# Kernel optimization log

Hardware: AMD Instinct MI355X
Metric: run time of the kernel (lower is better)

## Reference

```python
import jax, jax.numpy as jnp
import numpy as np

N_NODES = 100000
N_FEATS = 512
HIDDEN = 64
NUM_SAMPLES = 5
NUM_CLASSES = 16
BATCH = 16384


def setup_inputs() -> dict:
    key = jax.random.key(0)
    k1, k2, k3, k4, k5, k6, k7 = jax.random.split(key, 7)
    nodes = jax.random.randint(k1, (BATCH,), 0, N_NODES, dtype=jnp.int64) if jax.config.jax_enable_x64 else jax.random.randint(k1, (BATCH,), 0, N_NODES, dtype=jnp.int32)
    neigh_idx = jax.random.randint(k2, (N_NODES, NUM_SAMPLES), 0, N_NODES, dtype=jnp.int32)
    features = jax.random.normal(k3, (N_NODES, N_FEATS), dtype=jnp.float32)
    # xavier-uniform style init
    def xavier(k, shape):
        fan_in, fan_out = shape[1], shape[0]
        lim = jnp.sqrt(6.0 / (fan_in + fan_out)).astype(jnp.float32)
        return jax.random.uniform(k, shape, jnp.float32, -lim, lim)
    w1 = xavier(k4, (HIDDEN, 2 * N_FEATS))      # enc1 weight
    w2 = xavier(k5, (HIDDEN, 2 * HIDDEN))       # enc2 weight
    w_cls = xavier(k6, (NUM_CLASSES, HIDDEN))   # classifier weight
    return {"features": features, "w1": w1, "w2": w2, "w_cls": w_cls,
            "nodes": nodes, "neigh_idx": neigh_idx}


def reference(features, w1, w2, w_cls, nodes, neigh_idx):
    # Layer 1 (enc1, gcn=False): concat(self, mean(sampled neighbors)) -> W1 -> ReLU
    # Computed for all nodes (superset of what torch computes lazily; same values).
    neigh1 = features[neigh_idx].mean(axis=1)                      # [N, F]
    h1 = jax.nn.relu(jnp.concatenate([features, neigh1], axis=1) @ w1.T)  # [N, H]
    # Layer 2 (enc2) on the query batch
    self2 = h1[nodes]                                              # [B, H]
    neigh2 = h1[neigh_idx[nodes]].mean(axis=1)                     # [B, H]
    h2 = jax.nn.relu(jnp.concatenate([self2, neigh2], axis=1) @ w2.T)     # [B, H]
    # scores = (w_cls @ h2.T).T == h2 @ w_cls.T
    return h2 @ w_cls.T                                            # [B, C]
```

## Files before the change

kernel.cpp:

```cpp
#include <hip/hip_runtime.h>
#include <hip/hip_bf16.h>

#define N_NODES 100000
#define N_FEATS 512
#define HIDDEN 64
#define NUM_SAMPLES 5
#define NUM_CLASSES 16
#define BATCH 16384

typedef __attribute__((ext_vector_type(8))) short bf16x8;
typedef __attribute__((ext_vector_type(8))) unsigned short u16x8;
typedef __attribute__((ext_vector_type(4))) float f32x4;

static __device__ __forceinline__ float bf2f(unsigned short s) {
    unsigned int u = ((unsigned int)s) << 16;
    return __builtin_bit_cast(float, u);
}
static __device__ __forceinline__ short f2bf(float v) {
    __hip_bfloat16 b = __float2bfloat16(v);
    return *reinterpret_cast<short*>(&b);
}
static __device__ __forceinline__ int clampi(int v) {
    return ((unsigned)v < (unsigned)N_NODES) ? v : 0;
}

__global__ __launch_bounds__(256) void prep(const float* __restrict__ w1f,
                                            short* __restrict__ w1p,
                                            const int* __restrict__ nodes_i32,
                                            int* __restrict__ flag) {
    const int t = blockIdx.x * 256 + threadIdx.x;
    if (t < 64 * 1024) {
        const int j = t & 7;
        const int lane = (t >> 3) & 63;
        const int nb = (t >> 9) & 7;
        const int kk = t >> 12;
        const int l16 = lane & 15, quad = lane >> 4;
        const int cn = nb * 16 + l16;
        const int h = cn & 63, part = cn >> 6;
        w1p[t] = f2bf(w1f[h * 1024 + part * 512 + kk * 32 + quad * 8 + j]);
    }
    if (blockIdx.x == 0 && threadIdx.x == 0) {
        int odd_nonzero = 0;
        for (int i = 0; i < 64; i++)
            if (nodes_i32[2 * i + 1] != 0) odd_nonzero++;
        *flag = (odd_nonzero == 0) ? 1 : 0;
    }
}

__global__ __launch_bounds__(256) void pq_gemm(const float* __restrict__ feat,
                                               const short* __restrict__ w1p,
                                               short* __restrict__ PQ) {
    const int wave = threadIdx.x >> 6;
    const int lane = threadIdx.x & 63;
    const int quad = lane >> 4;
    const int l16  = lane & 15;
    const int r0   = blockIdx.x * 64 + wave * 16;

    int rA = r0 + l16;
    if (rA >= N_NODES) rA = N_NODES - 1;

    const float* aptr = feat + (size_t)rA * N_FEATS + quad * 8;
    const short* bbase = w1p + lane * 8;

    f32x4 buf[2][8];
#pragma unroll
    for (int c = 0; c < 4; c++) {
        buf[0][2 * c]     = *reinterpret_cast<const f32x4*>(aptr + c * 32);
        buf[0][2 * c + 1] = *reinterpret_cast<const f32x4*>(aptr + c * 32 + 4);
    }

    f32x4 acc[8];
#pragma unroll
    for (int i = 0; i < 8; i++) acc[i] = (f32x4){0.f, 0.f, 0.f, 0.f};

#pragma unroll
    for (int g = 0; g < 4; g++) {
        const int cur = g & 1;
        if (g < 3) {
#pragma unroll
            for (int c = 0; c < 4; c++) {
                buf[cur ^ 1][2 * c]     = *reinterpret_cast<const f32x4*>(aptr + (g + 1) * 128 + c * 32);
                buf[cur ^ 1][2 * c + 1] = *reinterpret_cast<const f32x4*>(aptr + (g + 1) * 128 + c * 32 + 4);
            }
        }
#pragma unroll
        for (int kk2 = 0; kk2 < 4; kk2++) {
            const int kk = g * 4 + kk2;
            bf16x8 afrag;
#pragma unroll
            for (int j = 0; j < 4; j++) {
                afrag[j]     = f2bf(buf[cur][2 * kk2][j]);
                afrag[4 + j] = f2bf(buf[cur][2 * kk2 + 1][j]);
            }
            const short* bk = bbase + kk * 4096;
#pragma unroll
            for (int nb = 0; nb < 8; nb++) {
                bf16x8 bfrag = *reinterpret_cast<const bf16x8*>(bk + nb * 512);
                acc[nb] = __builtin_amdgcn_mfma_f32_16x16x32_bf16(afrag, bfrag, acc[nb], 0, 0, 0);
            }
        }
    }

#pragma unroll
    for (int nb = 0; nb < 8; nb++) {
        const int cn = nb * 16 + l16;
#pragma unroll
        for (int r = 0; r < 4; r++) {
            const int row = r0 + quad * 4 + r;
            if (row < N_NODES) PQ[(size_t)row * 128 + cn] = f2bf(acc[nb][r]);
        }
    }
}

__global__ __launch_bounds__(256) void h1_combine(short* __restrict__ PQ,
                                                  const int* __restrict__ neigh_idx) {
    const int t = blockIdx.x * 256 + threadIdx.x;
    const int n = t >> 3;
    const int sub = t & 7;
    if (n >= N_NODES) return;

    u16x8 pv = *reinterpret_cast<const u16x8*>(PQ + (size_t)n * 128 + sub * 8);
    float s[8];
#pragma unroll
    for (int j = 0; j < 8; j++) s[j] = 0.f;
#pragma unroll
    for (int i = 0; i < NUM_SAMPLES; i++) {
        const int ni = clampi(neigh_idx[n * NUM_SAMPLES + i]);
        u16x8 qv = *reinterpret_cast<const u16x8*>(PQ + (size_t)ni * 128 + 64 + sub * 8);
#pragma unroll
        for (int j = 0; j < 8; j++) s[j] += bf2f(qv[j]);
    }
    u16x8 ov;
#pragma unroll
    for (int j = 0; j < 8; j++) {
        float v = bf2f(pv[j]) + 0.2f * s[j];
        v = v > 0.f ? v : 0.f;
        ov[j] = (unsigned short)f2bf(v);
    }
    *reinterpret_cast<u16x8*>(PQ + (size_t)n * 128 + sub * 8) = ov;
}

__global__ __launch_bounds__(256) void layer2_cls(const short* __restrict__ PQ,
                                                  const int* __restrict__ nodes_i32,
                                                  const int* __restrict__ neigh_idx,
                                                  const float* __restrict__ w2,
                                                  const float* __restrict__ wcls,
                                                  const int* __restrict__ flag,
                                                  float* __restrict__ out) {
    __shared__ float gbuf[16][128];
    __shared__ float h2buf[16][64];
    const int wave = threadIdx.x >> 6;
    const int lane = threadIdx.x & 63;
    const int is64 = *flag;
    const int b0 = blockIdx.x * 16;

#pragma unroll
    for (int it = 0; it < 4; it++) {
        const int item = wave * 4 + it;
        const int b = b0 + item;
        const int node = clampi(nodes_i32[is64 ? 2 * b : b]);
        float selfv = bf2f((unsigned short)PQ[(size_t)node * 128 + lane]);
        float ns = 0.f;
#pragma unroll
        for (int s = 0; s < NUM_SAMPLES; s++) {
            const int ni = clampi(neigh_idx[node * NUM_SAMPLES + s]);
            ns += bf2f((unsigned short)PQ[(size_t)ni * 128 + lane]);
        }
        gbuf[item][lane] = selfv;
        gbuf[item][64 + lane] = 0.2f * ns;
    }
    __syncthreads();

    float acc[4] = {0.f, 0.f, 0.f, 0.f};
    const f32x4* w2r = reinterpret_cast<const f32x4*>(w2 + lane * 128);
#pragma unroll 8
    for (int k = 0; k < 32; k++) {
        f32x4 w = w2r[k];
#pragma unroll
        for (int it = 0; it < 4; it++) {
            f32x4 g = *reinterpret_cast<const f32x4*>(&gbuf[wave * 4 + it][k * 4]);
            acc[it] += g[0] * w[0] + g[1] * w[1] + g[2] * w[2] + g[3] * w[3];
        }
    }
#pragma unroll
    for (int it = 0; it < 4; it++) {
        float h2 = acc[it] > 0.f ? acc[it] : 0.f;
        h2buf[wave * 4 + it][lane] = h2;
    }
    __syncthreads();

    if (lane < NUM_CLASSES) {
        const f32x4* wcr = reinterpret_cast<const f32x4*>(wcls + lane * 64);
#pragma unroll
        for (int it = 0; it < 4; it++) {
            const int item = wave * 4 + it;
            const f32x4* hr = reinterpret_cast<const f32x4*>(&h2buf[item][0]);
            float o = 0.f;
#pragma unroll
            for (int k = 0; k < 16; k++) {
                f32x4 h = hr[k], w = wcr[k];
                o += h[0] * w[0] + h[1] * w[1] + h[2] * w[2] + h[3] * w[3];
            }
            out[(size_t)(b0 + item) * NUM_CLASSES + lane] = o;
        }
    }
}

extern "C" void kernel_launch(void* const* d_in, const int* in_sizes, int n_in,
                              void* d_out, int out_size, void* d_ws, size_t ws_size,
                              hipStream_t stream) {
    const float* feat = nullptr;
    const float* w1 = nullptr;
    const float* w2 = nullptr;
    const float* wcls = nullptr;
    const int* nodes = nullptr;
    const int* neigh_idx = nullptr;
    for (int i = 0; i < n_in; i++) {
        switch (in_sizes[i]) {
            case 51200000: feat = (const float*)d_in[i]; break;
            case 65536:    w1 = (const float*)d_in[i]; break;
            case 8192:     w2 = (const float*)d_in[i]; break;
            case 1024:     wcls = (const float*)d_in[i]; break;
            case 16384:    nodes = (const int*)d_in[i]; break;
            case 500000:   neigh_idx = (const int*)d_in[i]; break;
            default: break;
        }
    }
    float* out = (float*)d_out;

    int* flag = (int*)d_ws;
    short* w1p = (short*)((char*)d_ws + 256);
    short* PQ  = (short*)((char*)d_ws + 256 + 64 * 1024 * sizeof(short));

    prep<<<256, 256, 0, stream>>>(w1, w1p, nodes, flag);
    pq_gemm<<<(N_NODES + 63) / 64, 256, 0, stream>>>(feat, w1p, PQ);
    h1_combine<<<(N_NODES * 8 + 255) / 256, 256, 0, stream>>>(PQ, neigh_idx);
    layer2_cls<<<BATCH / 16, 256, 0, stream>>>(PQ, nodes, neigh_idx, w2, wcls, flag, out);
}
```

Before: 368.6 us.

## Stage feature rows through swizzled LDS for coalesced loads in pq_gemm

```diff
diff --git a/kernel.cpp b/kernel.cpp
--- a/kernel.cpp
+++ b/kernel.cpp
@@ -50,49 +50,61 @@
 __global__ __launch_bounds__(256) void pq_gemm(const float* __restrict__ feat,
                                                const short* __restrict__ w1p,
                                                short* __restrict__ PQ) {
+    __shared__ short atile[4][16][256];
     const int wave = threadIdx.x >> 6;
     const int lane = threadIdx.x & 63;
     const int quad = lane >> 4;
     const int l16  = lane & 15;
     const int r0   = blockIdx.x * 64 + wave * 16;
 
-    int rA = r0 + l16;
-    if (rA >= N_NODES) rA = N_NODES - 1;
-
-    const float* aptr = feat + (size_t)rA * N_FEATS + quad * 8;
-    const short* bbase = w1p + lane * 8;
-
-    f32x4 buf[2][8];
-#pragma unroll
-    for (int c = 0; c < 4; c++) {
-        buf[0][2 * c]     = *reinterpret_cast<const f32x4*>(aptr + c * 32);
-        buf[0][2 * c + 1] = *reinterpret_cast<const f32x4*>(aptr + c * 32 + 4);
-    }
+    short* at = &atile[wave][0][0];
 
     f32x4 acc[8];
 #pragma unroll
     for (int i = 0; i < 8; i++) acc[i] = (f32x4){0.f, 0.f, 0.f, 0.f};
 
-#pragma unroll
-    for (int g = 0; g < 4; g++) {
-        const int cur = g & 1;
-        if (g < 3) {
-#pragma unroll
-            for (int c = 0; c < 4; c++) {
-                buf[cur ^ 1][2 * c]     = *reinterpret_cast<const f32x4*>(aptr + (g + 1) * 128 + c * 32);
-                buf[cur ^ 1][2 * c + 1] = *reinterpret_cast<const f32x4*>(aptr + (g + 1) * 128 + c * 32 + 4);
+    for (int kh = 0; kh < 2; kh++) {
+        f32x4 buf[2][4];
+
+#define ISSUE_GRP(g, slot)                                                        \
+        {                                                                         \
+            _Pragma("unroll")                                                     \
+            for (int j = 0; j < 4; j++) {                                         \
+                int rA = r0 + (g) * 4 + j;                                        \
+                if (rA >= N_NODES) rA = N_NODES - 1;                              \
+                buf[slot][j] = *reinterpret_cast<const f32x4*>(                   \
+                    feat + (size_t)rA * N_FEATS + kh * 256 + lane * 4);           \
+            }                                                                     \
+        }
+
+        ISSUE_GRP(0, 0)
+        ISSUE_GRP(1, 1)
+#pragma unroll
+        for (int g = 0; g < 4; g++) {
+            const int slot = g & 1;
+#pragma unroll
+            for (int j = 0; j < 4; j++) {
+                const int r = g * 4 + j;
+                f32x4 v = buf[slot][j];
+                unsigned long long pk =
+                      (unsigned long long)(unsigned short)f2bf(v[0])
+                    | ((unsigned long long)(unsigned short)f2bf(v[1]) << 16)
+                    | ((unsigned long long)(unsigned short)f2bf(v[2]) << 32)
+                    | ((unsigned long long)(unsigned short)f2bf(v[3]) << 48);
+                const int chunk = (lane >> 1) ^ (r & 7);
+                *reinterpret_cast<unsigned long long*>(
+                    at + r * 256 + chunk * 8 + (lane & 1) * 4) = pk;
             }
-        }
-#pragma unroll
-        for (int kk2 = 0; kk2 < 4; kk2++) {
-            const int kk = g * 4 + kk2;
-            bf16x8 afrag;
-#pragma unroll
-            for (int j = 0; j < 4; j++) {
-                afrag[j]     = f2bf(buf[cur][2 * kk2][j]);
-                afrag[4 + j] = f2bf(buf[cur][2 * kk2 + 1][j]);
-            }
-            const short* bk = bbase + kk * 4096;
+            if (g < 2) ISSUE_GRP(g + 2, slot)
+        }
+#undef ISSUE_GRP
+
+#pragma unroll
+        for (int kk = 0; kk < 8; kk++) {
+            const int chunk = kk * 4 + quad;
+            const int cs = chunk ^ (l16 & 7);
+            bf16x8 afrag = *reinterpret_cast<const bf16x8*>(at + l16 * 256 + cs * 8);
+            const short* bk = w1p + (size_t)(kh * 8 + kk) * 4096 + lane * 8;
 #pragma unroll
             for (int nb = 0; nb < 8; nb++) {
                 bf16x8 bfrag = *reinterpret_cast<const bf16x8*>(bk + nb * 512);
```

Measured after the change: 360.6 us. 1.02x faster.
